# Optimization experiments

Hardware: AMD Instinct MI355X
Metric: run time of the kernel (lower is better)

Reference implementation:

```python
import jax, jax.numpy as jnp
import numpy as np

N_HEADS = 8
D_HEAD = 64
INNER = N_HEADS * D_HEAD  # 512
D_X = 512
D_CTX = 768

def setup_inputs() -> dict:
    key = jax.random.key(0)
    ks = jax.random.split(key, 7)
    x = jax.random.normal(ks[0], (4, 4096, D_X), dtype=jnp.float32)
    context = jax.random.normal(ks[1], (4, 1024, D_CTX), dtype=jnp.float32)
    # Glorot-ish scaled params
    Wq = jax.random.normal(ks[2], (D_X, INNER), dtype=jnp.float32) / np.sqrt(D_X)
    Wk = jax.random.normal(ks[3], (D_CTX, INNER), dtype=jnp.float32) / np.sqrt(D_CTX)
    Wv = jax.random.normal(ks[4], (D_CTX, INNER), dtype=jnp.float32) / np.sqrt(D_CTX)
    Wo = jax.random.normal(ks[5], (INNER, INNER), dtype=jnp.float32) / np.sqrt(INNER)
    bo = jnp.zeros((INNER,), dtype=jnp.float32)
    return {"x": x, "context": context, "Wq": Wq, "Wk": Wk, "Wv": Wv, "Wo": Wo, "bo": bo}

def reference(x, context, Wq, Wk, Wv, Wo, bo):
    B, Nq, _ = x.shape
    Nc = context.shape[1]
    scale = D_HEAD ** -0.5
    # QKV projections (no bias), reshape to heads: b s (h d) -> b h s d
    q = (x @ Wq).reshape(B, Nq, N_HEADS, D_HEAD).transpose(0, 2, 1, 3)
    k = (context @ Wk).reshape(B, Nc, N_HEADS, D_HEAD).transpose(0, 2, 1, 3)
    v = (context @ Wv).reshape(B, Nc, N_HEADS, D_HEAD).transpose(0, 2, 1, 3)
    # scores: [B, H, Nq, Nc]
    score = jnp.einsum('bhqd,bhkd->bhqk', q, k) * scale
    weights = jax.nn.softmax(score, axis=-1)
    attn = jnp.einsum('bhqk,bhkd->bhqd', weights, v)
    out = attn.transpose(0, 2, 1, 3).reshape(B, Nq, INNER)
    return out @ Wo + bo
```

## Files before the change

kernel.cpp:

```cpp
#include <hip/hip_runtime.h>
#include <math.h>

typedef __attribute__((ext_vector_type(8))) short s8v;
typedef __attribute__((ext_vector_type(4))) float f4v;
typedef unsigned short u16;
typedef unsigned int u32;

constexpr int Bsz = 4, NQ = 4096, NC = 1024, NH = 8, DH = 64, DI = 512, DC = 768, DKV = 1024;

__device__ __forceinline__ u16 f2bf(float f) {
  union { float f; u32 u; } v; v.f = f;
  u32 r = v.u + 0x7fff + ((v.u >> 16) & 1);
  return (u16)(r >> 16);
}

__device__ __forceinline__ u32 pack2(float a, float b) {
  union { float f; u32 u; } ua, ub; ua.f = a; ub.f = b;
#if __has_builtin(__builtin_amdgcn_perm)
  return __builtin_amdgcn_perm(ub.u + 0x8000u, ua.u + 0x8000u, 0x07060302u);
#else
  return ((ub.u + 0x8000u) & 0xffff0000u) | ((ua.u + 0x8000u) >> 16);
#endif
}

#if __has_builtin(__builtin_amdgcn_exp2f)
#define EXP2(x) __builtin_amdgcn_exp2f(x)
#else
#define EXP2(x) exp2f(x)
#endif

__device__ __forceinline__ void g2l16(const void* g, void* l) {
  __builtin_amdgcn_global_load_lds((const __attribute__((address_space(1))) u32*)g,
                                   (__attribute__((address_space(3))) u32*)l, 16, 0, 0);
}

__global__ __launch_bounds__(256) void prep(const float* __restrict__ x, const float* __restrict__ ctx,
                                            const float* __restrict__ Wq, const float* __restrict__ Wk,
                                            const float* __restrict__ Wv, const float* __restrict__ Wo,
                                            u16* __restrict__ xb, u16* __restrict__ cb,
                                            u16* __restrict__ wqT, u16* __restrict__ wkvT,
                                            u16* __restrict__ woT) {
  int bx = blockIdx.x;
  if (bx < 11264) {
    const int NX4 = Bsz * NQ * DI / 4;
    const int NC4 = Bsz * NC * DC / 4;
    int i = bx * 256 + threadIdx.x;
    float4 v; u16* dst; int j;
    if (i < NX4) { v = ((const float4*)x)[i]; dst = xb; j = i; }
    else { j = i - NX4; if (j >= NC4) return; v = ((const float4*)ctx)[j]; dst = cb; }
    ushort4 o; o.x = f2bf(v.x); o.y = f2bf(v.y); o.z = f2bf(v.z); o.w = f2bf(v.w);
    ((ushort4*)dst)[j] = o;
    return;
  }
  int idx = bx - 11264;
  int z = idx / 96, rem = idx % 96, kx = rem % 12, ny = rem / 12;
  const float* src; u16* dst; int K; const int N = 512;
  if (z == 0)      { src = Wq; dst = wqT;              K = 512; }
  else if (z == 1) { src = Wk; dst = wkvT;             K = 768; }
  else if (z == 2) { src = Wv; dst = wkvT + 512 * 768; K = 768; }
  else             { src = Wo; dst = woT;              K = 512; }
  int k0 = kx * 64, n0 = ny * 64;
  if (k0 >= K) return;
  __shared__ u16 t[64][65];
  int tid = threadIdx.x, jr = tid & 63, ir = tid >> 6;
  for (int it = 0; it < 16; ++it) { int i = it * 4 + ir; t[i][jr] = f2bf(src[(size_t)(k0 + i) * N + n0 + jr]); }
  __syncthreads();
  for (int it = 0; it < 16; ++it) { int i = it * 4 + ir; dst[(size_t)(n0 + i) * K + k0 + jr] = t[jr][i]; }
}

__global__ __launch_bounds__(256) void vtrans(const u16* __restrict__ KVb, u16* __restrict__ Vt) {
  __shared__ u16 t[64][65];
  int t0 = blockIdx.x * 64, h = blockIdx.y, b = blockIdx.z;
  int tid = threadIdx.x, jr = tid & 63, ir = tid >> 6;
  for (int it = 0; it < 16; ++it) {
    int i = it * 4 + ir;
    t[i][jr] = KVb[((size_t)b * NC + t0 + i) * DKV + 512 + h * DH + jr];
  }
  __syncthreads();
  int perm = (jr & 32) + (((jr & 15) >> 2) << 3) + (((jr >> 4) & 1) << 2) + (jr & 3);
  for (int it = 0; it < 16; ++it) {
    int i = it * 4 + ir;
    Vt[((size_t)(b * NH + h) * DH + i) * NC + t0 + perm] = t[jr][i];
  }
}

template <bool F32OUT>
__device__ __forceinline__ void gemm_body(const u16* __restrict__ A, const u16* __restrict__ Bt,
                                          float* __restrict__ Cf, u16* __restrict__ Cb,
                                          const float* __restrict__ bias, int N, int K,
                                          float oscale, int nbx, int mby,
                                          u16* Al, u16* Bl) {
  int mb = mby * 128, nb = nbx * 128;
  int tid = threadIdx.x, lane = tid & 63, quad = lane >> 4, l16 = lane & 15, wave = tid >> 6;
  int wm = (wave >> 1) * 64, wn = (wave & 1) * 64;
  f4v acc[4][4];
  #pragma unroll
  for (int i = 0; i < 4; i++)
    #pragma unroll
    for (int j = 0; j < 4; j++) acc[i][j] = (f4v){0.f, 0.f, 0.f, 0.f};

  int r0 = tid >> 2, c0 = (tid & 3) * 8;
  const u16* Ap0 = A + (size_t)(mb + r0) * K + c0;
  const u16* Ap1 = A + (size_t)(mb + r0 + 64) * K + c0;
  const u16* Bp0 = Bt + (size_t)(nb + r0) * K + c0;
  const u16* Bp1 = Bt + (size_t)(nb + r0 + 64) * K + c0;

#define GSTAGE(k0, buf) do { \
    u16* al_ = Al + (buf) * 4096; u16* bl_ = Bl + (buf) * 4096; \
    g2l16(Ap0 + (k0), al_ + tid * 8); \
    g2l16(Ap1 + (k0), al_ + (tid + 256) * 8); \
    g2l16(Bp0 + (k0), bl_ + tid * 8); \
    g2l16(Bp1 + (k0), bl_ + (tid + 256) * 8); } while (0)

  GSTAGE(0, 0);
  int nk = K >> 5;
  for (int t = 0; t < nk; ++t) {
    __syncthreads();
    if (t + 1 < nk) GSTAGE((t + 1) * 32, (t + 1) & 1);
    const u16* al = Al + (t & 1) * 4096;
    const u16* bl = Bl + (t & 1) * 4096;
    s8v af[4], bfr[4];
    #pragma unroll
    for (int i = 0; i < 4; i++) af[i] = *(const s8v*)(al + (wm + i * 16 + l16) * 32 + quad * 8);
    #pragma unroll
    for (int j = 0; j < 4; j++) bfr[j] = *(const s8v*)(bl + (wn + j * 16 + l16) * 32 + quad * 8);
    #pragma unroll
    for (int i = 0; i < 4; i++)
      #pragma unroll
      for (int j = 0; j < 4; j++)
        acc[i][j] = __builtin_amdgcn_mfma_f32_16x16x32_bf16(af[i], bfr[j], acc[i][j], 0, 0, 0);
  }
#undef GSTAGE
  #pragma unroll
  for (int i = 0; i < 4; i++) {
    int rbase = mb + wm + i * 16 + quad * 4;
    #pragma unroll
    for (int j = 0; j < 4; j++) {
      int col = nb + wn + j * 16 + l16;
      #pragma unroll
      for (int r = 0; r < 4; r++) {
        size_t idx = (size_t)(rbase + r) * N + col;
        if (F32OUT) Cf[idx] = acc[i][j][r] * oscale + bias[col];
        else        Cb[idx] = f2bf(acc[i][j][r] * oscale);
      }
    }
  }
}

__global__ __launch_bounds__(256, 3) void proj_all(const u16* __restrict__ xb, const u16* __restrict__ cb,
                                                   const u16* __restrict__ wqT, const u16* __restrict__ wkvT,
                                                   u16* __restrict__ Qb, u16* __restrict__ KVb,
                                                   float qscale) {
  __shared__ alignas(16) u16 Al[2][128][32];
  __shared__ alignas(16) u16 Bl[2][128][32];
  int bx = blockIdx.x;
  if (bx < 512) {
    gemm_body<false>(xb, wqT, nullptr, Qb, nullptr, 512, 512, qscale, bx & 3, bx >> 2,
                     (u16*)Al, (u16*)Bl);
  } else {
    int bi = bx - 512;
    gemm_body<false>(cb, wkvT, nullptr, KVb, nullptr, 1024, 768, 1.0f, bi & 7, bi >> 3,
                     (u16*)Al, (u16*)Bl);
  }
}

__global__ __launch_bounds__(256, 3) void outproj(const u16* __restrict__ Ob, const u16* __restrict__ woT,
                                                  float* __restrict__ out, const float* __restrict__ bo) {
  __shared__ alignas(16) u16 Al[2][128][32];
  __shared__ alignas(16) u16 Bl[2][128][32];
  gemm_body<true>(Ob, woT, out, nullptr, bo, 512, 512, 1.0f, blockIdx.x, blockIdx.y,
                  (u16*)Al, (u16*)Bl);
}

__global__ __launch_bounds__(256, 2) void attn(const u16* __restrict__ Q, const u16* __restrict__ KVb,
                                               const u16* __restrict__ Vt, u16* __restrict__ O) {
  __shared__ alignas(16) u16 Kl[2][64][64];
  __shared__ alignas(16) u16 Vl[2][64][64];
  int qt = blockIdx.x, h = blockIdx.y, b = blockIdx.z;
  int tid = threadIdx.x, wave = tid >> 6, lane = tid & 63, quad = lane >> 4, l16 = lane & 15;
  int q0 = qt * 256 + wave * 64;
  int x7 = l16 & 7;

  int s1 = tid + 256;
  int kr0 = tid >> 3, kc0 = (tid & 7) ^ (kr0 & 7);
  int kr1 = s1 >> 3,  kc1 = (s1 & 7) ^ (kr1 & 7);
  const u16* kg0 = KVb + ((size_t)b * NC + kr0) * DKV + h * DH + kc0 * 8;
  const u16* kg1 = KVb + ((size_t)b * NC + kr1) * DKV + h * DH + kc1 * 8;
  const u16* vg0 = Vt + ((size_t)(b * NH + h) * DH + kr0) * NC + kc0 * 8;
  const u16* vg1 = Vt + ((size_t)(b * NH + h) * DH + kr1) * NC + kc1 * 8;

#define ASTAGE(kt, buf) do { \
    size_t ko_ = (size_t)(kt) * 64 * DKV; int vo_ = (kt) * 64; \
    g2l16(kg0 + ko_, (u16*)Kl + (buf) * 4096 + tid * 8); \
    g2l16(kg1 + ko_, (u16*)Kl + (buf) * 4096 + (tid + 256) * 8); \
    g2l16(vg0 + vo_, (u16*)Vl + (buf) * 4096 + tid * 8); \
    g2l16(vg1 + vo_, (u16*)Vl + (buf) * 4096 + (tid + 256) * 8); } while (0)

  s8v aq[4][2];
  {
    const u16* Qp = Q + ((size_t)b * NQ + q0 + l16) * DI + h * DH + quad * 8;
    #pragma unroll
    for (int n = 0; n < 4; n++) {
      aq[n][0] = *(const s8v*)(Qp + (size_t)n * 16 * DI);
      aq[n][1] = *(const s8v*)(Qp + (size_t)n * 16 * DI + 32);
    }
  }
  f4v oacc[4][4];
  float lsum[4] = {0.f, 0.f, 0.f, 0.f};
  #pragma unroll
  for (int d = 0; d < 4; d++)
    #pragma unroll
    for (int n = 0; n < 4; n++) oacc[d][n] = (f4v){0.f, 0.f, 0.f, 0.f};

  ASTAGE(0, 0);
  for (int kt = 0; kt < NC / 64; ++kt) {
    int buf = kt & 1;
    __syncthreads();
    if (kt + 1 < NC / 64) ASTAGE(kt + 1, buf ^ 1);
    const u16* kb = (const u16*)Kl + buf * 4096;
    const u16* vb = (const u16*)Vl + buf * 4096;

    #pragma unroll
    for (int c = 0; c < 2; c++) {
      f4v S[2][4];
      #pragma unroll
      for (int mi = 0; mi < 2; mi++)
        #pragma unroll
        for (int n = 0; n < 4; n++) S[mi][n] = (f4v){0.f, 0.f, 0.f, 0.f};
      #pragma unroll
      for (int cd = 0; cd < 2; cd++) {
        int rA = 32 * c + l16;
        int ch = ((4 * cd + quad) ^ x7) * 8;
        s8v kf0 = *(const s8v*)(kb + rA * 64 + ch);
        s8v kf1 = *(const s8v*)(kb + (rA + 16) * 64 + ch);
        #pragma unroll
        for (int n = 0; n < 4; n++) {
          S[0][n] = __builtin_amdgcn_mfma_f32_16x16x32_bf16(kf0, aq[n][cd], S[0][n], 0, 0, 0);
          S[1][n] = __builtin_amdgcn_mfma_f32_16x16x32_bf16(kf1, aq[n][cd], S[1][n], 0, 0, 0);
        }
      }
      s8v pf[4];
      #pragma unroll
      for (int n = 0; n < 4; n++) {
        float p00 = EXP2(S[0][n][0]), p01 = EXP2(S[0][n][1]), p02 = EXP2(S[0][n][2]), p03 = EXP2(S[0][n][3]);
        float p10 = EXP2(S[1][n][0]), p11 = EXP2(S[1][n][1]), p12 = EXP2(S[1][n][2]), p13 = EXP2(S[1][n][3]);
        lsum[n] += (p00 + p01) + (p02 + p03) + (p10 + p11) + (p12 + p13);
        union { u32 d[4]; s8v v; } u;
        u.d[0] = pack2(p00, p01); u.d[1] = pack2(p02, p03);
        u.d[2] = pack2(p10, p11); u.d[3] = pack2(p12, p13);
        pf[n] = u.v;
      }
      #pragma unroll
      for (int d = 0; d < 4; d++) {
        int rV = d * 16 + l16;
        int ch = ((4 * c + quad) ^ x7) * 8;
        s8v vf = *(const s8v*)(vb + rV * 64 + ch);
        #pragma unroll
        for (int n = 0; n < 4; n++)
          oacc[d][n] = __builtin_amdgcn_mfma_f32_16x16x32_bf16(vf, pf[n], oacc[d][n], 0, 0, 0);
      }
    }
  }
#undef ASTAGE

  float inv[4];
  #pragma unroll
  for (int n = 0; n < 4; n++) {
    float s = lsum[n];
    s += __shfl_xor(s, 16); s += __shfl_xor(s, 32);
    inv[n] = 1.0f / s;
  }
  #pragma unroll
  for (int d = 0; d < 4; d++)
    #pragma unroll
    for (int n = 0; n < 4; n++) {
      int q = q0 + n * 16 + l16;
      uint2 ov;
      ov.x = pack2(oacc[d][n][0] * inv[n], oacc[d][n][1] * inv[n]);
      ov.y = pack2(oacc[d][n][2] * inv[n], oacc[d][n][3] * inv[n]);
      *(uint2*)(O + ((size_t)b * NQ + q) * DI + h * DH + d * 16 + quad * 4) = ov;
    }
}

extern "C" void kernel_launch(void* const* d_in, const int* in_sizes, int n_in,
                              void* d_out, int out_size, void* d_ws, size_t ws_size,
                              hipStream_t stream) {
  const float* x   = (const float*)d_in[0];
  const float* ctx = (const float*)d_in[1];
  const float* Wq  = (const float*)d_in[2];
  const float* Wk  = (const float*)d_in[3];
  const float* Wv  = (const float*)d_in[4];
  const float* Wo  = (const float*)d_in[5];
  const float* bo  = (const float*)d_in[6];
  float* out = (float*)d_out;

  u16* w    = (u16*)d_ws;
  u16* xb   = w;
  u16* cb   = xb   + 8388608;
  u16* wqT  = cb   + 3145728;
  u16* wkvT = wqT  + 262144;
  u16* woT  = wkvT + 786432;
  u16* Qb   = woT  + 262144;
  u16* KVb  = Qb   + 8388608;
  u16* Vtb  = KVb  + 4194304;
  u16* Ob   = Vtb  + 2097152;

  const float qscale = 0.125f * 1.44269504f;

  prep<<<11648, 256, 0, stream>>>(x, ctx, Wq, Wk, Wv, Wo, xb, cb, wqT, wkvT, woT);
  proj_all<<<768, 256, 0, stream>>>(xb, cb, wqT, wkvT, Qb, KVb, qscale);
  vtrans<<<dim3(16, 8, 4), 256, 0, stream>>>(KVb, Vtb);
  attn<<<dim3(16, 8, 4), 256, 0, stream>>>(Qb, KVb, Vtb, Ob);
  outproj<<<dim3(4, 128), 256, 0, stream>>>(Ob, woT, out, bo);
}
```

Baseline: 193.4 us.

## Fuse V transpose into KV projection epilogue and shrink GEMM/attention tiles

```diff
diff --git a/kernel.cpp b/kernel.cpp
--- a/kernel.cpp
+++ b/kernel.cpp
@@ -6,7 +6,7 @@
 typedef unsigned short u16;
 typedef unsigned int u32;
 
-constexpr int Bsz = 4, NQ = 4096, NC = 1024, NH = 8, DH = 64, DI = 512, DC = 768, DKV = 1024;
+constexpr int Bsz = 4, NQ = 4096, NC = 1024, NH = 8, DH = 64, DI = 512, DC = 768;
 
 __device__ __forceinline__ u16 f2bf(float f) {
   union { float f; u32 u; } v; v.f = f;
@@ -68,49 +68,31 @@
   for (int it = 0; it < 16; ++it) { int i = it * 4 + ir; dst[(size_t)(n0 + i) * K + k0 + jr] = t[jr][i]; }
 }
 
-__global__ __launch_bounds__(256) void vtrans(const u16* __restrict__ KVb, u16* __restrict__ Vt) {
-  __shared__ u16 t[64][65];
-  int t0 = blockIdx.x * 64, h = blockIdx.y, b = blockIdx.z;
-  int tid = threadIdx.x, jr = tid & 63, ir = tid >> 6;
-  for (int it = 0; it < 16; ++it) {
-    int i = it * 4 + ir;
-    t[i][jr] = KVb[((size_t)b * NC + t0 + i) * DKV + 512 + h * DH + jr];
-  }
-  __syncthreads();
-  int perm = (jr & 32) + (((jr & 15) >> 2) << 3) + (((jr >> 4) & 1) << 2) + (jr & 3);
-  for (int it = 0; it < 16; ++it) {
-    int i = it * 4 + ir;
-    Vt[((size_t)(b * NH + h) * DH + i) * NC + t0 + perm] = t[jr][i];
-  }
-}
-
-template <bool F32OUT>
+template <int MODE>
 __device__ __forceinline__ void gemm_body(const u16* __restrict__ A, const u16* __restrict__ Bt,
-                                          float* __restrict__ Cf, u16* __restrict__ Cb,
+                                          void* __restrict__ C0, void* __restrict__ C1,
                                           const float* __restrict__ bias, int N, int K,
                                           float oscale, int nbx, int mby,
                                           u16* Al, u16* Bl) {
-  int mb = mby * 128, nb = nbx * 128;
+  int mb = mby * 128, nb = nbx * 64;
   int tid = threadIdx.x, lane = tid & 63, quad = lane >> 4, l16 = lane & 15, wave = tid >> 6;
-  int wm = (wave >> 1) * 64, wn = (wave & 1) * 64;
-  f4v acc[4][4];
+  int wm = (wave >> 1) * 64, wn = (wave & 1) * 32;
+  f4v acc[4][2];
   #pragma unroll
   for (int i = 0; i < 4; i++)
     #pragma unroll
-    for (int j = 0; j < 4; j++) acc[i][j] = (f4v){0.f, 0.f, 0.f, 0.f};
+    for (int j = 0; j < 2; j++) acc[i][j] = (f4v){0.f, 0.f, 0.f, 0.f};
 
   int r0 = tid >> 2, c0 = (tid & 3) * 8;
   const u16* Ap0 = A + (size_t)(mb + r0) * K + c0;
   const u16* Ap1 = A + (size_t)(mb + r0 + 64) * K + c0;
   const u16* Bp0 = Bt + (size_t)(nb + r0) * K + c0;
-  const u16* Bp1 = Bt + (size_t)(nb + r0 + 64) * K + c0;
 
 #define GSTAGE(k0, buf) do { \
-    u16* al_ = Al + (buf) * 4096; u16* bl_ = Bl + (buf) * 4096; \
+    u16* al_ = Al + (buf) * 4096; u16* bl_ = Bl + (buf) * 2048; \
     g2l16(Ap0 + (k0), al_ + tid * 8); \
     g2l16(Ap1 + (k0), al_ + (tid + 256) * 8); \
-    g2l16(Bp0 + (k0), bl_ + tid * 8); \
-    g2l16(Bp1 + (k0), bl_ + (tid + 256) * 8); } while (0)
+    g2l16(Bp0 + (k0), bl_ + tid * 8); } while (0)
 
   GSTAGE(0, 0);
   int nk = K >> 5;
@@ -118,16 +100,16 @@
     __syncthreads();
     if (t + 1 < nk) GSTAGE((t + 1) * 32, (t + 1) & 1);
     const u16* al = Al + (t & 1) * 4096;
-    const u16* bl = Bl + (t & 1) * 4096;
-    s8v af[4], bfr[4];
+    const u16* bl = Bl + (t & 1) * 2048;
+    s8v af[4], bfr[2];
     #pragma unroll
     for (int i = 0; i < 4; i++) af[i] = *(const s8v*)(al + (wm + i * 16 + l16) * 32 + quad * 8);
     #pragma unroll
-    for (int j = 0; j < 4; j++) bfr[j] = *(const s8v*)(bl + (wn + j * 16 + l16) * 32 + quad * 8);
+    for (int j = 0; j < 2; j++) bfr[j] = *(const s8v*)(bl + (wn + j * 16 + l16) * 32 + quad * 8);
     #pragma unroll
     for (int i = 0; i < 4; i++)
       #pragma unroll
-      for (int j = 0; j < 4; j++)
+      for (int j = 0; j < 2; j++)
         acc[i][j] = __builtin_amdgcn_mfma_f32_16x16x32_bf16(af[i], bfr[j], acc[i][j], 0, 0, 0);
   }
 #undef GSTAGE
@@ -135,66 +117,84 @@
   for (int i = 0; i < 4; i++) {
     int rbase = mb + wm + i * 16 + quad * 4;
     #pragma unroll
-    for (int j = 0; j < 4; j++) {
+    for (int j = 0; j < 2; j++) {
       int col = nb + wn + j * 16 + l16;
-      #pragma unroll
-      for (int r = 0; r < 4; r++) {
-        size_t idx = (size_t)(rbase + r) * N + col;
-        if (F32OUT) Cf[idx] = acc[i][j][r] * oscale + bias[col];
-        else        Cb[idx] = f2bf(acc[i][j][r] * oscale);
+      if (MODE == 0) {
+        u16* Cb = (u16*)C0;
+        #pragma unroll
+        for (int r = 0; r < 4; r++) Cb[(size_t)(rbase + r) * N + col] = f2bf(acc[i][j][r] * oscale);
+      } else if (MODE == 1) {
+        float* Cf = (float*)C0;
+        #pragma unroll
+        for (int r = 0; r < 4; r++) Cf[(size_t)(rbase + r) * N + col] = acc[i][j][r] + bias[col];
+      } else {
+        if (nbx < 8) {
+          u16* Kb = (u16*)C0;
+          #pragma unroll
+          for (int r = 0; r < 4; r++) Kb[(size_t)(rbase + r) * 512 + col] = f2bf(acc[i][j][r]);
+        } else {
+          u16* Vt = (u16*)C1;
+          int hd = col - 512, h = hd >> 6, d = hd & 63;
+          int bb = rbase >> 10, tl = rbase & 1023;
+          int tbase = tl & ~63, a0 = tl & 63;
+          int pb = (a0 & 32) + ((a0 & 15) >> 2) * 8 + (((a0 >> 4) & 1) << 2);
+          uint2 ov;
+          ov.x = pack2(acc[i][j][0], acc[i][j][1]);
+          ov.y = pack2(acc[i][j][2], acc[i][j][3]);
+          *(uint2*)(Vt + ((size_t)(bb * NH + h) * DH + d) * NC + tbase + pb) = ov;
+        }
       }
     }
   }
 }
 
-__global__ __launch_bounds__(256, 3) void proj_all(const u16* __restrict__ xb, const u16* __restrict__ cb,
+__global__ __launch_bounds__(256, 4) void proj_all(const u16* __restrict__ xb, const u16* __restrict__ cb,
                                                    const u16* __restrict__ wqT, const u16* __restrict__ wkvT,
-                                                   u16* __restrict__ Qb, u16* __restrict__ KVb,
-                                                   float qscale) {
+                                                   u16* __restrict__ Qb, u16* __restrict__ Kb,
+                                                   u16* __restrict__ Vtb, float qscale) {
   __shared__ alignas(16) u16 Al[2][128][32];
-  __shared__ alignas(16) u16 Bl[2][128][32];
+  __shared__ alignas(16) u16 Bl[2][64][32];
   int bx = blockIdx.x;
-  if (bx < 512) {
-    gemm_body<false>(xb, wqT, nullptr, Qb, nullptr, 512, 512, qscale, bx & 3, bx >> 2,
-                     (u16*)Al, (u16*)Bl);
+  if (bx < 1024) {
+    gemm_body<0>(xb, wqT, Qb, nullptr, nullptr, 512, 512, qscale, bx & 7, bx >> 3,
+                 (u16*)Al, (u16*)Bl);
   } else {
-    int bi = bx - 512;
-    gemm_body<false>(cb, wkvT, nullptr, KVb, nullptr, 1024, 768, 1.0f, bi & 7, bi >> 3,
-                     (u16*)Al, (u16*)Bl);
-  }
-}
-
-__global__ __launch_bounds__(256, 3) void outproj(const u16* __restrict__ Ob, const u16* __restrict__ woT,
+    int bi = bx - 1024;
+    gemm_body<2>(cb, wkvT, Kb, Vtb, nullptr, 1024, 768, 1.0f, bi & 15, bi >> 4,
+                 (u16*)Al, (u16*)Bl);
+  }
+}
+
+__global__ __launch_bounds__(256, 4) void outproj(const u16* __restrict__ Ob, const u16* __restrict__ woT,
                                                   float* __restrict__ out, const float* __restrict__ bo) {
   __shared__ alignas(16) u16 Al[2][128][32];
-  __shared__ alignas(16) u16 Bl[2][128][32];
-  gemm_body<true>(Ob, woT, out, nullptr, bo, 512, 512, 1.0f, blockIdx.x, blockIdx.y,
-                  (u16*)Al, (u16*)Bl);
-}
-
-__global__ __launch_bounds__(256, 2) void attn(const u16* __restrict__ Q, const u16* __restrict__ KVb,
+  __shared__ alignas(16) u16 Bl[2][64][32];
+  gemm_body<1>(Ob, woT, out, nullptr, bo, 512, 512, 1.0f, blockIdx.x, blockIdx.y,
+               (u16*)Al, (u16*)Bl);
+}
+
+__global__ __launch_bounds__(128, 2) void attn(const u16* __restrict__ Q, const u16* __restrict__ Kb,
                                                const u16* __restrict__ Vt, u16* __restrict__ O) {
   __shared__ alignas(16) u16 Kl[2][64][64];
   __shared__ alignas(16) u16 Vl[2][64][64];
   int qt = blockIdx.x, h = blockIdx.y, b = blockIdx.z;
   int tid = threadIdx.x, wave = tid >> 6, lane = tid & 63, quad = lane >> 4, l16 = lane & 15;
-  int q0 = qt * 256 + wave * 64;
+  int q0 = qt * 128 + wave * 64;
   int x7 = l16 & 7;
 
-  int s1 = tid + 256;
-  int kr0 = tid >> 3, kc0 = (tid & 7) ^ (kr0 & 7);
-  int kr1 = s1 >> 3,  kc1 = (s1 & 7) ^ (kr1 & 7);
-  const u16* kg0 = KVb + ((size_t)b * NC + kr0) * DKV + h * DH + kc0 * 8;
-  const u16* kg1 = KVb + ((size_t)b * NC + kr1) * DKV + h * DH + kc1 * 8;
-  const u16* vg0 = Vt + ((size_t)(b * NH + h) * DH + kr0) * NC + kc0 * 8;
-  const u16* vg1 = Vt + ((size_t)(b * NH + h) * DH + kr1) * NC + kc1 * 8;
+  int kr = tid >> 3, kc = (tid & 7) ^ (kr & 7);
+  const u16* kg = Kb + ((size_t)b * NC + kr) * 512 + h * DH + kc * 8;
+  const u16* vg = Vt + ((size_t)(b * NH + h) * DH + kr) * NC + kc * 8;
 
 #define ASTAGE(kt, buf) do { \
-    size_t ko_ = (size_t)(kt) * 64 * DKV; int vo_ = (kt) * 64; \
-    g2l16(kg0 + ko_, (u16*)Kl + (buf) * 4096 + tid * 8); \
-    g2l16(kg1 + ko_, (u16*)Kl + (buf) * 4096 + (tid + 256) * 8); \
-    g2l16(vg0 + vo_, (u16*)Vl + (buf) * 4096 + tid * 8); \
-    g2l16(vg1 + vo_, (u16*)Vl + (buf) * 4096 + (tid + 256) * 8); } while (0)
+    const u16* kg_ = kg + (size_t)(kt) * 64 * 512; \
+    const u16* vg_ = vg + (kt) * 64; \
+    u16* kl_ = (u16*)Kl + (buf) * 4096; u16* vl_ = (u16*)Vl + (buf) * 4096; \
+    _Pragma("unroll") \
+    for (int it = 0; it < 4; ++it) { \
+      g2l16(kg_ + (size_t)it * 16 * 512, kl_ + (tid + it * 128) * 8); \
+      g2l16(vg_ + (size_t)it * 16 * NC,  vl_ + (tid + it * 128) * 8); \
+    } } while (0)
 
   s8v aq[4][2];
   {
@@ -301,15 +301,14 @@
   u16* wkvT = wqT  + 262144;
   u16* woT  = wkvT + 786432;
   u16* Qb   = woT  + 262144;
-  u16* KVb  = Qb   + 8388608;
-  u16* Vtb  = KVb  + 4194304;
+  u16* Kbuf = Qb   + 8388608;
+  u16* Vtb  = Kbuf + 2097152;
   u16* Ob   = Vtb  + 2097152;
 
   const float qscale = 0.125f * 1.44269504f;
 
   prep<<<11648, 256, 0, stream>>>(x, ctx, Wq, Wk, Wv, Wo, xb, cb, wqT, wkvT, woT);
-  proj_all<<<768, 256, 0, stream>>>(xb, cb, wqT, wkvT, Qb, KVb, qscale);
-  vtrans<<<dim3(16, 8, 4), 256, 0, stream>>>(KVb, Vtb);
-  attn<<<dim3(16, 8, 4), 256, 0, stream>>>(Qb, KVb, Vtb, Ob);
-  outproj<<<dim3(4, 128), 256, 0, stream>>>(Ob, woT, out, bo);
-}
+  proj_all<<<1536, 256, 0, stream>>>(xb, cb, wqT, wkvT, Qb, Kbuf, Vtb, qscale);
+  attn<<<dim3(32, 8, 4), 128, 0, stream>>>(Qb, Kbuf, Vtb, Ob);
+  outproj<<<dim3(8, 128), 256, 0, stream>>>(Ob, woT, out, bo);
+}
```

Measured after the change: 207.5 us. 1.07x slower.
